# Kernel optimization log

Hardware: AMD Instinct MI355X
Metric: run time of the kernel (lower is better)

## Reference

```python
import jax, jax.numpy as jnp
import numpy as np
from jax.scipy.linalg import solve_triangular

B, T, HID = 1, 2048, 2048
HK, DK = 16, 96
HV, DV = 16, 192
KDIM, VDIM = HK * DK, HV * DV
KCONV = 4
CHUNK = 64
EPS = 1e-6


def setup_inputs():
    key = jax.random.key(0)
    ks = jax.random.split(key, 16)
    s = 0.02
    return {
        "hidden_states": jax.random.normal(ks[0], (B, T, HID), jnp.float32),
        "Wq": jax.random.normal(ks[1], (HID, KDIM), jnp.float32) * s,
        "Wk": jax.random.normal(ks[2], (HID, KDIM), jnp.float32) * s,
        "Wv": jax.random.normal(ks[3], (HID, VDIM), jnp.float32) * s,
        "Wb": jax.random.normal(ks[4], (HID, HV), jnp.float32) * s,
        "Wa": jax.random.normal(ks[5], (HID, HV), jnp.float32) * s,
        "Wg": jax.random.normal(ks[6], (HID, VDIM), jnp.float32) * s,
        "Wo": jax.random.normal(ks[7], (VDIM, HID), jnp.float32) * s,
        "conv_q": jax.random.normal(ks[8], (KDIM, KCONV), jnp.float32) * 0.5,
        "conv_k": jax.random.normal(ks[9], (KDIM, KCONV), jnp.float32) * 0.5,
        "conv_v": jax.random.normal(ks[10], (VDIM, KCONV), jnp.float32) * 0.5,
        "A_log": jnp.log(jax.random.uniform(ks[11], (HV,), jnp.float32, 1.0, 16.0)),
        "dt_bias": jax.random.uniform(ks[12], (HV,), jnp.float32, 0.0, 1.0),
        "norm_weight": jnp.ones((DV,), jnp.float32),
    }


def short_conv_silu(x, w):
    # x: [B,T,C], w: [C,K]; causal depthwise conv (left pad K-1) then SiLU
    K = w.shape[-1]
    xp = jnp.pad(x, ((0, 0), (K - 1, 0), (0, 0)))
    y = sum(xp[:, j:j + x.shape[1], :] * w[:, j] for j in range(K))
    return jax.nn.silu(y)


def l2norm(x):
    return x * jax.lax.rsqrt(jnp.sum(x * x, axis=-1, keepdims=True) + EPS)


def chunk_gated_delta_rule(q, k, v, g, beta):
    # q,k: [B,T,H,dk]; v: [B,T,H,dv]; g,beta: [B,T,H]. Chunked parallel scan (WY form).
    Bb, Tt, H, dk = q.shape
    dv = v.shape[-1]
    N = Tt // CHUNK
    q = l2norm(q) * (dk ** -0.5)
    k = l2norm(k)
    chunk = lambda x: x.transpose(0, 2, 1, 3).reshape(Bb, H, N, CHUNK, x.shape[-1])
    qc, kc, vc = chunk(q), chunk(k), chunk(v)
    gc = jnp.cumsum(g.transpose(0, 2, 1).reshape(Bb, H, N, CHUNK), axis=-1)
    bc = beta.transpose(0, 2, 1).reshape(Bb, H, N, CHUNK)

    m_inc = jnp.tril(jnp.ones((CHUNK, CHUNK), bool))
    m_str = jnp.tril(jnp.ones((CHUNK, CHUNK), bool), -1)
    diff = gc[..., :, None] - gc[..., None, :]
    D = jnp.exp(jnp.where(m_inc, diff, 0.0)) * m_inc  # [B,H,N,C,C] intra-chunk decay

    kb = kc * bc[..., None]
    A = -jnp.einsum('bhnik,bhnjk->bhnij', kb, kc) * D * m_str
    eye = jnp.eye(CHUNK, dtype=q.dtype)
    # UT transform: Tm = (I - A)^{-1}, A strictly lower triangular
    Tm = solve_triangular(eye - A, jnp.broadcast_to(eye, A.shape), lower=True, unit_diagonal=True)
    u = Tm @ (vc * bc[..., None])                   # [B,H,N,C,dv]
    w = Tm @ (kb * jnp.exp(gc)[..., None])          # [B,H,N,C,dk]
    g_last = gc[..., -1]                            # [B,H,N]

    def step(S, inp):
        q_i, k_i, u_i, w_i, g_i, D_i, gl = inp
        v_new = u_i - w_i @ S                       # [B,H,C,dv]
        attn = jnp.einsum('bhik,bhjk->bhij', q_i, k_i) * D_i
        o_i = (q_i * jnp.exp(g_i)[..., None]) @ S + attn @ v_new
        k_dec = k_i * jnp.exp(gl[..., None] - g_i)[..., None]
        S = S * jnp.exp(gl)[..., None, None] + jnp.einsum('bhck,bhcv->bhkv', k_dec, v_new)
        return S, o_i

    mv = lambda x: jnp.moveaxis(x, 2, 0)
    S0 = jnp.zeros((Bb, H, dk, dv), q.dtype)
    _, o = jax.lax.scan(step, S0, (mv(qc), mv(kc), mv(u), mv(w), mv(gc), mv(D), mv(g_last)))
    o = jnp.moveaxis(o, 0, 2).reshape(Bb, H, Tt, dv)
    return o.transpose(0, 2, 1, 3)                  # [B,T,H,dv]


def reference(hidden_states, Wq, Wk, Wv, Wb, Wa, Wg, Wo, conv_q, conv_k, conv_v, A_log, dt_bias, norm_weight):
    q = short_conv_silu(hidden_states @ Wq, conv_q).reshape(B, T, HK, DK)
    k = short_conv_silu(hidden_states @ Wk, conv_k).reshape(B, T, HK, DK)
    v = short_conv_silu(hidden_states @ Wv, conv_v).reshape(B, T, HV, DV)
    beta = jax.nn.sigmoid(hidden_states @ Wb) * 2.0          # allow_neg_eigval -> beta in [0,2]
    g = -jnp.exp(A_log) * jax.nn.softplus(hidden_states @ Wa + dt_bias)  # log decay, [B,T,HV]
    o = chunk_gated_delta_rule(q, k, v, g, beta)             # [B,T,HV,DV]
    gate = (hidden_states @ Wg).reshape(B, T, HV, DV)
    o = o * jax.nn.silu(gate)                                # gated RMSNorm (gate, then norm)
    o = o * jax.lax.rsqrt(jnp.mean(o * o, axis=-1, keepdims=True) + EPS) * norm_weight
    return o.reshape(B, T, VDIM) @ Wo
```

## Files before the change

### kernel.cpp

```cpp
#include <hip/hip_runtime.h>
#include <math.h>

#define T_LEN 2048
#define HIDN  2048
#define HKN   16
#define DKN   96
#define HVN   16
#define DVN   192
#define KDIMN 1536
#define VDIMN 3072
#define QKVD  6144
#define CHUNKN 64
#define NCHUNK 32
#define EPSF 1e-6f
#define TN_STRIDE 10240

typedef __attribute__((ext_vector_type(8))) short short8;
typedef __attribute__((ext_vector_type(4))) float f32x4;

__device__ __forceinline__ unsigned short f2bf(float f) {
    unsigned int u = __float_as_uint(f);
    unsigned int r = (u + 0x7FFFu + ((u >> 16) & 1u)) >> 16;
    return (unsigned short)r;
}
__device__ __forceinline__ float bf2f(unsigned short u) {
    return __uint_as_float(((unsigned int)u) << 16);
}
__device__ __forceinline__ float siluf(float x) { return x / (1.f + expf(-x)); }

__device__ __forceinline__ void gld_lds16(const void* g, void* l) {
    __builtin_amdgcn_global_load_lds((const __attribute__((address_space(1))) unsigned int*)g,
                                     (__attribute__((address_space(3))) unsigned int*)l, 16, 0, 0);
}

__global__ void cast_f32_bf16(const float* __restrict__ in, unsigned short* __restrict__ out, int n) {
    int i = (blockIdx.x * blockDim.x + threadIdx.x) * 4;
    if (i >= n) return;
    float4 v = *(const float4*)(in + i);
    ushort4 o;
    o.x = f2bf(v.x); o.y = f2bf(v.y); o.z = f2bf(v.z); o.w = f2bf(v.w);
    *(ushort4*)(out + i) = o;
}

__global__ void prep_weights(const float* __restrict__ Wq, const float* __restrict__ Wk,
                             const float* __restrict__ Wv, const float* __restrict__ Wg,
                             const float* __restrict__ Wo,
                             unsigned short* __restrict__ WallT, unsigned short* __restrict__ WoT) {
    __shared__ float tile[64][65];
    int bid = blockIdx.x;
    const float* W; unsigned short* Wt; int K, N, l;
    if (bid < 768)       { W = Wq; Wt = WallT;                          K = 2048; N = 1536; l = bid; }
    else if (bid < 1536) { W = Wk; Wt = WallT + (size_t)1536 * 2048;    K = 2048; N = 1536; l = bid - 768; }
    else if (bid < 3072) { W = Wv; Wt = WallT + (size_t)3072 * 2048;    K = 2048; N = 3072; l = bid - 1536; }
    else if (bid < 4608) { W = Wg; Wt = WallT + (size_t)6144 * 2048;    K = 2048; N = 3072; l = bid - 3072; }
    else                 { W = Wo; Wt = WoT;                            K = 3072; N = 2048; l = bid - 4608; }
    int nbx = N >> 6;
    int n0 = (l % nbx) * 64, k0 = (l / nbx) * 64;
    int tx = threadIdx.x, ty = threadIdx.y;
    for (int r = ty; r < 64; r += 4) tile[r][tx] = W[(size_t)(k0 + r) * N + n0 + tx];
    __syncthreads();
    for (int r = ty; r < 64; r += 4) Wt[(size_t)(n0 + r) * K + k0 + tx] = f2bf(tile[tx][r]);
}

__global__ __launch_bounds__(256) void gemm_bt2(const unsigned short* __restrict__ A,
                                                const unsigned short* __restrict__ Bt,
                                                float* __restrict__ C1, int ld1, int nblk1,
                                                unsigned short* __restrict__ C2, int ld2,
                                                int M, int K) {
    __shared__ __align__(16) unsigned short As[2][128 * 32];
    __shared__ __align__(16) unsigned short Bs[2][128 * 32];
    int tid = threadIdx.x;
    int wave = tid >> 6, lane = tid & 63;
    int bm = blockIdx.y, bn = blockIdx.x;
    f32x4 acc[4][4] = {};
    int wr = wave >> 1, wc = wave & 1;
    int rstage = wave * 32 + (lane >> 2);
    int cstage = (lane & 3) * 8;
    const size_t a_row0 = (size_t)bm * 128;
    const size_t b_row0 = (size_t)bn * 128;
    const unsigned short* gaBase = A + (a_row0 + rstage) * (size_t)K + cstage;
    const unsigned short* gbBase = Bt + (b_row0 + rstage) * (size_t)K + cstage;
    int row_a[4], row_b[4];
#pragma unroll
    for (int i = 0; i < 4; ++i) {
        row_a[i] = wr * 64 + i * 16 + (lane & 15);
        row_b[i] = wc * 64 + i * 16 + (lane & 15);
    }
    int koff = (lane >> 4) * 8;
    int niter = K >> 5;
    {
        unsigned short* ab = &As[0][wave * 1024];
        unsigned short* bb = &Bs[0][wave * 1024];
        gld_lds16(gaBase, ab);
        gld_lds16(gaBase + (size_t)16 * K, ab + 512);
        gld_lds16(gbBase, bb);
        gld_lds16(gbBase + (size_t)16 * K, bb + 512);
    }
    __syncthreads();
    for (int i = 0; i < niter; ++i) {
        int cur = i & 1;
        if (i + 1 < niter) {
            int k0 = (i + 1) * 32;
            unsigned short* ab = &As[cur ^ 1][wave * 1024];
            unsigned short* bb = &Bs[cur ^ 1][wave * 1024];
            gld_lds16(gaBase + k0, ab);
            gld_lds16(gaBase + k0 + (size_t)16 * K, ab + 512);
            gld_lds16(gbBase + k0, bb);
            gld_lds16(gbBase + k0 + (size_t)16 * K, bb + 512);
        }
        short8 af[4], bfr[4];
#pragma unroll
        for (int mi = 0; mi < 4; ++mi) af[mi] = *(const short8*)&As[cur][row_a[mi] * 32 + koff];
#pragma unroll
        for (int ni = 0; ni < 4; ++ni) bfr[ni] = *(const short8*)&Bs[cur][row_b[ni] * 32 + koff];
#pragma unroll
        for (int mi = 0; mi < 4; ++mi)
#pragma unroll
            for (int ni = 0; ni < 4; ++ni)
                acc[mi][ni] = __builtin_amdgcn_mfma_f32_16x16x32_bf16(af[mi], bfr[ni], acc[mi][ni], 0, 0, 0);
        __syncthreads();
    }
    if (bn < nblk1) {
        int colb = bn * 128;
#pragma unroll
        for (int mi = 0; mi < 4; ++mi) {
            int rbase = bm * 128 + wr * 64 + mi * 16 + (lane >> 4) * 4;
#pragma unroll
            for (int ni = 0; ni < 4; ++ni) {
                int col = colb + wc * 64 + ni * 16 + (lane & 15);
#pragma unroll
                for (int j = 0; j < 4; ++j)
                    C1[(size_t)(rbase + j) * ld1 + col] = acc[mi][ni][j];
            }
        }
    } else {
        int colb = (bn - nblk1) * 128;
#pragma unroll
        for (int mi = 0; mi < 4; ++mi) {
            int rbase = bm * 128 + wr * 64 + mi * 16 + (lane >> 4) * 4;
#pragma unroll
            for (int ni = 0; ni < 4; ++ni) {
                int col = colb + wc * 64 + ni * 16 + (lane & 15);
#pragma unroll
                for (int j = 0; j < 4; ++j)
                    C2[(size_t)(rbase + j) * ld2 + col] = f2bf(acc[mi][ni][j]);
            }
        }
    }
}

__global__ __launch_bounds__(256) void gemm_btk(const unsigned short* __restrict__ A,
                                                const unsigned short* __restrict__ Bt,
                                                float* __restrict__ C, float* __restrict__ Cp,
                                                int M, int N, int K) {
    __shared__ __align__(16) unsigned short As[2][128 * 32];
    __shared__ __align__(16) unsigned short Bs[2][128 * 32];
    int tid = threadIdx.x;
    int wave = tid >> 6, lane = tid & 63;
    int bm = blockIdx.y, bn = blockIdx.x, kz = blockIdx.z;
    int kchunk = K / 3;
    int kbeg = kz * kchunk;
    f32x4 acc[4][4] = {};
    int wr = wave >> 1, wc = wave & 1;
    int rstage = wave * 32 + (lane >> 2);
    int cstage = (lane & 3) * 8;
    const size_t a_row0 = (size_t)bm * 128;
    const size_t b_row0 = (size_t)bn * 128;
    const unsigned short* gaBase = A + (a_row0 + rstage) * (size_t)K + kbeg + cstage;
    const unsigned short* gbBase = Bt + (b_row0 + rstage) * (size_t)K + kbeg + cstage;
    int row_a[4], row_b[4];
#pragma unroll
    for (int i = 0; i < 4; ++i) {
        row_a[i] = wr * 64 + i * 16 + (lane & 15);
        row_b[i] = wc * 64 + i * 16 + (lane & 15);
    }
    int koff = (lane >> 4) * 8;
    int niter = kchunk >> 5;
    {
        unsigned short* ab = &As[0][wave * 1024];
        unsigned short* bb = &Bs[0][wave * 1024];
        gld_lds16(gaBase, ab);
        gld_lds16(gaBase + (size_t)16 * K, ab + 512);
        gld_lds16(gbBase, bb);
        gld_lds16(gbBase + (size_t)16 * K, bb + 512);
    }
    __syncthreads();
    for (int i = 0; i < niter; ++i) {
        int cur = i & 1;
        if (i + 1 < niter) {
            int k0 = (i + 1) * 32;
            unsigned short* ab = &As[cur ^ 1][wave * 1024];
            unsigned short* bb = &Bs[cur ^ 1][wave * 1024];
            gld_lds16(gaBase + k0, ab);
            gld_lds16(gaBase + k0 + (size_t)16 * K, ab + 512);
            gld_lds16(gbBase + k0, bb);
            gld_lds16(gbBase + k0 + (size_t)16 * K, bb + 512);
        }
        short8 af[4], bfr[4];
#pragma unroll
        for (int mi = 0; mi < 4; ++mi) af[mi] = *(const short8*)&As[cur][row_a[mi] * 32 + koff];
#pragma unroll
        for (int ni = 0; ni < 4; ++ni) bfr[ni] = *(const short8*)&Bs[cur][row_b[ni] * 32 + koff];
#pragma unroll
        for (int mi = 0; mi < 4; ++mi)
#pragma unroll
            for (int ni = 0; ni < 4; ++ni)
                acc[mi][ni] = __builtin_amdgcn_mfma_f32_16x16x32_bf16(af[mi], bfr[ni], acc[mi][ni], 0, 0, 0);
        __syncthreads();
    }
    float* Cout = (kz == 0) ? C : (Cp + (size_t)(kz - 1) * M * N);
#pragma unroll
    for (int mi = 0; mi < 4; ++mi) {
        int rbase = bm * 128 + wr * 64 + mi * 16 + (lane >> 4) * 4;
#pragma unroll
        for (int ni = 0; ni < 4; ++ni) {
            int col = bn * 128 + wc * 64 + ni * 16 + (lane & 15);
#pragma unroll
            for (int j = 0; j < 4; ++j)
                Cout[(size_t)(rbase + j) * N + col] = acc[mi][ni][j];
        }
    }
}

__global__ void addk(float* __restrict__ out, const float* __restrict__ p, int n) {
    int i = (blockIdx.x * blockDim.x + threadIdx.x) * 4;
    if (i >= n) return;
    float4 a = *(const float4*)(out + i);
    float4 b = *(const float4*)(p + i);
    float4 c = *(const float4*)(p + n + i);
    a.x += b.x + c.x; a.y += b.y + c.y; a.z += b.z + c.z; a.w += b.w + c.w;
    *(float4*)(out + i) = a;
}

__global__ __launch_bounds__(256) void beta_g(const float* __restrict__ X,
                                              const float* __restrict__ Wb, const float* __restrict__ Wa,
                                              const float* __restrict__ A_log, const float* __restrict__ dtb,
                                              float* __restrict__ bvec, float* __restrict__ gvec) {
    int t = blockIdx.x;
    int tid = threadIdx.x;
    int cg = tid & 7, ks = tid >> 3;
    int wave = tid >> 6, lane = tid & 63;
    const float* xr = X + (size_t)t * HIDN;
    const float* Wsel = (cg < 4) ? Wb : Wa;
    int cc = (cg & 3) * 4;
    float ax = 0.f, ay = 0.f, az = 0.f, aw = 0.f;
#pragma unroll 4
    for (int i = 0; i < 16; ++i) {
        int k = (ks + 32 * i) * 4;
        float4 xv = *(const float4*)(xr + k);
        float4 w0 = *(const float4*)(Wsel + (size_t)(k + 0) * 16 + cc);
        float4 w1 = *(const float4*)(Wsel + (size_t)(k + 1) * 16 + cc);
        float4 w2 = *(const float4*)(Wsel + (size_t)(k + 2) * 16 + cc);
        float4 w3 = *(const float4*)(Wsel + (size_t)(k + 3) * 16 + cc);
        ax += xv.x * w0.x + xv.y * w1.x + xv.z * w2.x + xv.w * w3.x;
        ay += xv.x * w0.y + xv.y * w1.y + xv.z * w2.y + xv.w * w3.y;
        az += xv.x * w0.z + xv.y * w1.z + xv.z * w2.z + xv.w * w3.z;
        aw += xv.x * w0.w + xv.y * w1.w + xv.z * w2.w + xv.w * w3.w;
    }
#pragma unroll
    for (int off = 8; off <= 32; off <<= 1) {
        ax += __shfl_xor(ax, off, 64);
        ay += __shfl_xor(ay, off, 64);
        az += __shfl_xor(az, off, 64);
        aw += __shfl_xor(aw, off, 64);
    }
    __shared__ float red[4][8][4];
    if ((lane >> 3) == 0) {
        red[wave][cg][0] = ax; red[wave][cg][1] = ay;
        red[wave][cg][2] = az; red[wave][cg][3] = aw;
    }
    __syncthreads();
    if (tid < 8) {
        float tot[4];
#pragma unroll
        for (int j = 0; j < 4; ++j)
            tot[j] = red[0][tid][j] + red[1][tid][j] + red[2][tid][j] + red[3][tid][j];
        int c0 = (tid & 3) * 4;
        if (tid < 4) {
#pragma unroll
            for (int j = 0; j < 4; ++j)
                bvec[(size_t)t * 16 + c0 + j] = 2.f / (1.f + expf(-tot[j]));
        } else {
#pragma unroll
            for (int j = 0; j < 4; ++j) {
                float a = tot[j] + dtb[c0 + j];
                float sp = (a > 20.f) ? a : log1pf(expf(a));
                gvec[(size_t)t * 16 + c0 + j] = -expf(A_log[c0 + j]) * sp;
            }
        }
    }
}

__global__ __launch_bounds__(256) void phase1_mfma(
    const float* __restrict__ Cqkv,
    const float* __restrict__ cq, const float* __restrict__ ck, const float* __restrict__ cv,
    const float* __restrict__ gvec, const float* __restrict__ bvec,
    float* __restrict__ u_ws, float* __restrict__ w_ws,
    float* __restrict__ qg_ws, float* __restrict__ at_ws,
    float* __restrict__ gl_ws, float* __restrict__ Ct,
    unsigned short* __restrict__ Tn) {
    int n = blockIdx.x, h = blockIdx.y;
    int t0 = n * CHUNKN;
    int tid = threadIdx.x;
    int wave = tid >> 6, lane = tid & 63;
    size_t base = (size_t)(h * NCHUNK + n);

    __shared__ __align__(16) char LB1[139776];
    unsigned short* QKb  = (unsigned short*)(LB1 + 0);
    unsigned short* Pb   = (unsigned short*)(LB1 + 26624);
    unsigned short* RHSw = (unsigned short*)(LB1 + 39936);
    unsigned short* RHSv = (unsigned short*)(LB1 + 53760);
    unsigned short* Ab   = (unsigned short*)(LB1 + 81408);
    unsigned short* Atb  = (unsigned short*)(LB1 + 94720);
    unsigned short* Ptb  = (unsigned short*)(LB1 + 108032);
    float*          Pf   = (float*)(LB1 + 121344);
    unsigned short* kdT  = (unsigned short*)(LB1 + 81408);
    unsigned short* wT   = (unsigned short*)(LB1 + 95232);
    unsigned short* uT   = (unsigned short*)(LB1 + 109056);
    float* gr_s = (float*)(LB1 + 138752);
    float* gc_s = gr_s + 64;
    float* be_s = gc_s + 64;
    float* egc  = be_s + 64;
    __shared__ __align__(16) float cwS[384 * 4];

    for (int f = tid; f < 384; f += 256) {
        const float* src = (f < 96)  ? (cq + (size_t)(h * 96 + f) * 4)
                         : (f < 192) ? (ck + (size_t)(h * 96 + f - 96) * 4)
                                     : (cv + (size_t)(h * 192 + f - 192) * 4);
        *(float4*)&cwS[f * 4] = *(const float4*)src;
    }
    if (tid < 64) {
        gr_s[tid] = gvec[(size_t)(t0 + tid) * HVN + h];
        be_s[tid] = bvec[(size_t)(t0 + tid) * HVN + h];
    }
    __syncthreads();
    if (tid < 64) {
        float sacc = 0.f;
        for (int j = 0; j <= tid; ++j) sacc += gr_s[j];
        gc_s[tid] = sacc;
    }
    __syncthreads();
    float gl = gc_s[63];
    if (tid < 64) egc[tid] = expf(gl - gc_s[tid]);

    int r = tid >> 2, sub = tid & 3;
    int trow = t0 + r;
    {
        int gc0 = 1536 + h * DKN + sub * 24;
        int lc0 = 96 + sub * 24;
        float kreg[24];
        float ss = 0.f;
#pragma unroll
        for (int i = 0; i < 6; ++i) {
            float4 x0 = (trow >= 3) ? *(const float4*)(Cqkv + (size_t)(trow - 3) * QKVD + gc0 + i * 4) : make_float4(0, 0, 0, 0);
            float4 x1 = (trow >= 2) ? *(const float4*)(Cqkv + (size_t)(trow - 2) * QKVD + gc0 + i * 4) : make_float4(0, 0, 0, 0);
            float4 x2 = (trow >= 1) ? *(const float4*)(Cqkv + (size_t)(trow - 1) * QKVD + gc0 + i * 4) : make_float4(0, 0, 0, 0);
            float4 x3 = *(const float4*)(Cqkv + (size_t)trow * QKVD + gc0 + i * 4);
#pragma unroll
            for (int c = 0; c < 4; ++c) {
                float4 w = *(const float4*)&cwS[(lc0 + i * 4 + c) * 4];
                float xv = ((const float*)&x0)[c] * w.x + ((const float*)&x1)[c] * w.y
                         + ((const float*)&x2)[c] * w.z + ((const float*)&x3)[c] * w.w;
                xv = siluf(xv);
                kreg[i * 4 + c] = xv;
                ss += xv * xv;
            }
        }
        ss += __shfl_xor(ss, 1, 64);
        ss += __shfl_xor(ss, 2, 64);
        float nrm = rsqrtf(ss + EPSF);
        float ebg = be_s[r] * expf(gc_s[r]);
#pragma unroll
        for (int i = 0; i < 24; ++i) {
            float kn = kreg[i] * nrm;
            QKb[r * 104 + sub * 24 + i] = f2bf(kn);
            RHSw[(sub * 24 + i) * 72 + r] = f2bf(kn * ebg);
        }
    }
    {
        int gc0 = h * DKN + sub * 24;
        int lc0 = sub * 24;
        float qreg[24];
        float ss = 0.f;
#pragma unroll
        for (int i = 0; i < 6; ++i) {
            float4 x0 = (trow >= 3) ? *(const float4*)(Cqkv + (size_t)(trow - 3) * QKVD + gc0 + i * 4) : make_float4(0, 0, 0, 0);
            float4 x1 = (trow >= 2) ? *(const float4*)(Cqkv + (size_t)(trow - 2) * QKVD + gc0 + i * 4) : make_float4(0, 0, 0, 0);
            float4 x2 = (trow >= 1) ? *(const float4*)(Cqkv + (size_t)(trow - 1) * QKVD + gc0 + i * 4) : make_float4(0, 0, 0, 0);
            float4 x3 = *(const float4*)(Cqkv + (size_t)trow * QKVD + gc0 + i * 4);
#pragma unroll
            for (int c = 0; c < 4; ++c) {
                float4 w = *(const float4*)&cwS[(lc0 + i * 4 + c) * 4];
                float xv = ((const float*)&x0)[c] * w.x + ((const float*)&x1)[c] * w.y
                         + ((const float*)&x2)[c] * w.z + ((const float*)&x3)[c] * w.w;
                xv = siluf(xv);
                qreg[i * 4 + c] = xv;
                ss += xv * xv;
            }
        }
        ss += __shfl_xor(ss, 1, 64);
        ss += __shfl_xor(ss, 2, 64);
        float nrm = rsqrtf(ss + EPSF) * 0.10206207261596577f;
        float eg = expf(gc_s[r]);
        float* qgp = qg_ws + base * (64 * 96) + r * 96 + sub * 24;
#pragma unroll
        for (int i = 0; i < 24; ++i) {
            float qn = qreg[i] * nrm;
            QKb[(64 + r) * 104 + sub * 24 + i] = f2bf(qn);
            qgp[i] = qn * eg;
        }
    }
    {
        int gc0 = 3072 + h * DVN + sub * 48;
        int lc0 = 192 + sub * 48;
        float ber = be_s[r];
#pragma unroll
        for (int i = 0; i < 12; ++i) {
            float4 x0 = (trow >= 3) ? *(const float4*)(Cqkv + (size_t)(trow - 3) * QKVD + gc0 + i * 4) : make_float4(0, 0, 0, 0);
            float4 x1 = (trow >= 2) ? *(const float4*)(Cqkv + (size_t)(trow - 2) * QKVD + gc0 + i * 4) : make_float4(0, 0, 0, 0);
            float4 x2 = (trow >= 1) ? *(const float4*)(Cqkv + (size_t)(trow - 1) * QKVD + gc0 + i * 4) : make_float4(0, 0, 0, 0);
            float4 x3 = *(const float4*)(Cqkv + (size_t)trow * QKVD + gc0 + i * 4);
#pragma unroll
            for (int c = 0; c < 4; ++c) {
                float4 w = *(const float4*)&cwS[(lc0 + i * 4 + c) * 4];
                float xv = ((const float*)&x0)[c] * w.x + ((const float*)&x1)[c] * w.y
                         + ((const float*)&x2)[c] * w.z + ((const float*)&x3)[c] * w.w;
                RHSv[(sub * 48 + i * 4 + c) * 72 + r] = f2bf(siluf(xv) * ber);
            }
        }
    }
    __syncthreads();

    {
        f32x4 acc1[2][4] = {};
#pragma unroll
        for (int ks = 0; ks < 3; ++ks) {
            int ko = ks * 32 + (lane >> 4) * 8;
            short8 af[2], bfv[4];
#pragma unroll
            for (int rt2 = 0; rt2 < 2; ++rt2)
                af[rt2] = *(const short8*)&QKb[(wave * 32 + rt2 * 16 + (lane & 15)) * 104 + ko];
#pragma unroll
            for (int ct = 0; ct < 4; ++ct)
                bfv[ct] = *(const short8*)&QKb[(ct * 16 + (lane & 15)) * 104 + ko];
#pragma unroll
            for (int rt2 = 0; rt2 < 2; ++rt2)
#pragma unroll
                for (int ct = 0; ct < 4; ++ct)
                    acc1[rt2][ct] = __builtin_amdgcn_mfma_f32_16x16x32_bf16(af[rt2], bfv[ct], acc1[rt2][ct], 0, 0, 0);
        }
#pragma unroll
        for (int rt2 = 0; rt2 < 2; ++rt2)
#pragma unroll
            for (int ct = 0; ct < 4; ++ct)
#pragma unroll
                for (int j = 0; j < 4; ++j) {
                    int rr = wave * 32 + rt2 * 16 + (lane >> 4) * 4 + j;
                    int cc = ct * 16 + (lane & 15);
                    float val = acc1[rt2][ct][j];
                    if (rr < 64) {
                        float av = (rr > cc) ? -be_s[rr] * expf(gc_s[rr] - gc_s[cc]) * val : 0.f;
                        unsigned short ab = f2bf(av);
                        Ab[rr * 104 + cc] = ab;
                        Atb[cc * 104 + rr] = ab;
                        float pv = (rr == cc) ? 1.f : av;
                        Pf[rr * 68 + cc] = pv;
                        unsigned short pb = f2bf(pv);
                        Pb[rr * 104 + cc] = pb;
                        Ptb[cc * 104 + rr] = pb;
                    } else {
                        int ar = rr - 64;
                        float av = (ar >= cc) ? expf(gc_s[ar] - gc_s[cc]) * val : 0.f;
                        at_ws[base * (64 * 64) + ar * 64 + cc] = av;
                    }
                }
    }
    __syncthreads();

#pragma unroll 1
    for (int lev = 0; lev < 5; ++lev) {
        f32x4 d[4] = {};
#pragma unroll
        for (int ks = 0; ks < 2; ++ks) {
            int ko = ks * 32 + (lane >> 4) * 8;
            short8 a0 = *(const short8*)&Ab[(wave * 16 + (lane & 15)) * 104 + ko];
#pragma unroll
            for (int ct = 0; ct < 4; ++ct) {
                short8 b0 = *(const short8*)&Atb[(ct * 16 + (lane & 15)) * 104 + ko];
                d[ct] = __builtin_amdgcn_mfma_f32_16x16x32_bf16(a0, b0, d[ct], 0, 0, 0);
            }
        }
        __syncthreads();
#pragma unroll
        for (int ct = 0; ct < 4; ++ct)
#pragma unroll
            for (int j = 0; j < 4; ++j) {
                int rr = wave * 16 + (lane >> 4) * 4 + j;
                int cc = ct * 16 + (lane & 15);
                unsigned short hb = f2bf(d[ct][j]);
                Ab[rr * 104 + cc] = hb;
                Atb[cc * 104 + rr] = hb;
            }
        __syncthreads();
        f32x4 e[4];
#pragma unroll
        for (int ct = 0; ct < 4; ++ct)
#pragma unroll
            for (int j = 0; j < 4; ++j)
                e[ct][j] = Pf[(wave * 16 + (lane >> 4) * 4 + j) * 68 + ct * 16 + (lane & 15)];
#pragma unroll
        for (int ks = 0; ks < 2; ++ks) {
            int ko = ks * 32 + (lane >> 4) * 8;
            short8 a0 = *(const short8*)&Ab[(wave * 16 + (lane & 15)) * 104 + ko];
#pragma unroll
            for (int ct = 0; ct < 4; ++ct) {
                short8 b0 = *(const short8*)&Ptb[(ct * 16 + (lane & 15)) * 104 + ko];
                e[ct] = __builtin_amdgcn_mfma_f32_16x16x32_bf16(a0, b0, e[ct], 0, 0, 0);
            }
        }
        __syncthreads();
#pragma unroll
        for (int ct = 0; ct < 4; ++ct)
#pragma unroll
            for (int j = 0; j < 4; ++j) {
                int rr = wave * 16 + (lane >> 4) * 4 + j;
                int cc = ct * 16 + (lane & 15);
                float pv = e[ct][j];
                Pf[rr * 68 + cc] = pv;
                unsigned short pb = f2bf(pv);
                Pb[rr * 104 + cc] = pb;
                Ptb[cc * 104 + rr] = pb;
            }
        __syncthreads();
    }

    for (int f = tid; f < 6144; f += 256) {
        int d = f >> 6, tt = f & 63;
        kdT[d * 72 + tt] = f2bf(bf2f(QKb[tt * 104 + d]) * egc[tt]);
    }

#pragma unroll 1
    for (int i = 0; i < 18; ++i) {
        int id = wave * 18 + i;
        int rt = id & 3, ct = id >> 2;
        f32x4 o4 = {};
#pragma unroll
        for (int ks = 0; ks < 2; ++ks) {
            int ko = ks * 32 + (lane >> 4) * 8;
            short8 a0 = *(const short8*)&Pb[(rt * 16 + (lane & 15)) * 104 + ko];
            short8 b0 = (ct < 12)
                ? *(const short8*)&RHSv[(ct * 16 + (lane & 15)) * 72 + ko]
                : *(const short8*)&RHSw[((ct - 12) * 16 + (lane & 15)) * 72 + ko];
            o4 = __builtin_amdgcn_mfma_f32_16x16x32_bf16(a0, b0, o4, 0, 0, 0);
        }
#pragma unroll
        for (int j = 0; j < 4; ++j) {
            int rr = rt * 16 + (lane >> 4) * 4 + j;
            int nn = ct * 16 + (lane & 15);
            if (ct < 12) {
                u_ws[base * (64 * 192) + rr * 192 + nn] = o4[j];
                uT[nn * 72 + rr] = f2bf(o4[j]);
            } else {
                w_ws[base * (64 * 96) + rr * 96 + (nn - 192)] = o4[j];
                wT[(nn - 192) * 72 + rr] = f2bf(o4[j]);
            }
        }
    }
    __syncthreads();

    float eglv = expf(gl);
#pragma unroll 1
    for (int q = 0; q < 27; ++q) {
        int id = wave * 27 + q;
        f32x4 acc = {};
        if (id < 36) {
            int jt = id / 6, kt = id % 6;
#pragma unroll
            for (int ks = 0; ks < 2; ++ks) {
                int ko = ks * 32 + (lane >> 4) * 8;
                short8 a0 = *(const short8*)&kdT[(jt * 16 + (lane & 15)) * 72 + ko];
                short8 b0 = *(const short8*)&wT[(kt * 16 + (lane & 15)) * 72 + ko];
                acc = __builtin_amdgcn_mfma_f32_16x16x32_bf16(a0, b0, acc, 0, 0, 0);
            }
#pragma unroll
            for (int rr = 0; rr < 4; ++rr) {
                int j = jt * 16 + (lane >> 4) * 4 + rr;
                int k = kt * 16 + (lane & 15);
                float val = -acc[rr];
                if (j == k) val += eglv;
                Tn[base * TN_STRIDE + j * 104 + k] = f2bf(val);
            }
        } else {
            int cid = id - 36;
            int it = cid / 6, jt = cid % 6;
#pragma unroll
            for (int ks = 0; ks < 2; ++ks) {
                int ko = ks * 32 + (lane >> 4) * 8;
                short8 a0 = *(const short8*)&uT[(it * 16 + (lane & 15)) * 72 + ko];
                short8 b0 = *(const short8*)&kdT[(jt * 16 + (lane & 15)) * 72 + ko];
                acc = __builtin_amdgcn_mfma_f32_16x16x32_bf16(a0, b0, acc, 0, 0, 0);
            }
#pragma unroll
            for (int rr = 0; rr < 4; ++rr)
                Ct[base * 18432 + (size_t)(it * 16 + (lane >> 4) * 4 + rr) * 96 + jt * 16 + (lane & 15)] = acc[rr];
        }
    }
    if (tid == 0) gl_ws[base] = gl;
}

__global__ __launch_bounds__(128) void mscan(const float* __restrict__ Ct, const unsigned short* __restrict__ Tn,
                                             float* __restrict__ s_ws) {
    int rg = blockIdx.x, h = blockIdx.y;
    int tid = threadIdx.x, wave = tid >> 6, lane = tid & 63;
    __shared__ __align__(16) unsigned short St[48 * 104];
    __shared__ __align__(16) unsigned short TnB[2][TN_STRIDE];
    __shared__ __align__(16) float CtB[2][48 * 96];
    for (int i = tid; i < 48 * 104; i += 128) St[i] = 0;

    {
        const float* cp = Ct + (size_t)(h * NCHUNK) * 18432 + rg * (48 * 96);
        const unsigned short* tp = Tn + (size_t)(h * NCHUNK) * TN_STRIDE;
#pragma unroll
        for (int q = 0; q < 9; ++q) {
            size_t o = (size_t)(wave * 9 + q) * 1024 + lane * 16;
            gld_lds16((const char*)cp + o, (char*)&CtB[0][0] + (size_t)(wave * 9 + q) * 1024);
        }
#pragma unroll
        for (int q = 0; q < 10; ++q) {
            size_t o = (size_t)(wave * 10 + q) * 1024 + lane * 16;
            gld_lds16((const char*)tp + o, (char*)&TnB[0][0] + (size_t)(wave * 10 + q) * 1024);
        }
    }
    f32x4 acc[3][3] = {};
    int colw = wave * 48;
    __syncthreads();

#pragma unroll 1
    for (int n = 0; n < NCHUNK; ++n) {
        size_t base = (size_t)(h * NCHUNK + n);
        int cur = n & 1;
        if (n + 1 < NCHUNK) {
            const float* cp = Ct + (base + 1) * 18432 + rg * (48 * 96);
            const unsigned short* tp = Tn + (base + 1) * TN_STRIDE;
#pragma unroll
            for (int q = 0; q < 9; ++q) {
                size_t o = (size_t)(wave * 9 + q) * 1024 + lane * 16;
                gld_lds16((const char*)cp + o, (char*)&CtB[cur ^ 1][0] + (size_t)(wave * 9 + q) * 1024);
            }
#pragma unroll
            for (int q = 0; q < 10; ++q) {
                size_t o = (size_t)(wave * 10 + q) * 1024 + lane * 16;
                gld_lds16((const char*)tp + o, (char*)&TnB[cur ^ 1][0] + (size_t)(wave * 10 + q) * 1024);
            }
        }
        float* sp = s_ws + base * 18432 + rg * (48 * 96);
#pragma unroll
        for (int it = 0; it < 3; ++it)
#pragma unroll
            for (int jt = 0; jt < 3; ++jt) {
                int irow = it * 16 + (lane >> 4) * 4;
                int col = colw + jt * 16 + (lane & 15);
#pragma unroll
                for (int r = 0; r < 4; ++r) {
                    sp[(size_t)(irow + r) * 96 + col] = acc[it][jt][r];
                    acc[it][jt][r] = CtB[cur][(irow + r) * 96 + col];
                }
            }
#pragma unroll
        for (int ks = 0; ks < 3; ++ks) {
            int ko = ks * 32 + (lane >> 4) * 8;
            short8 af[3], bfv[3];
#pragma unroll
            for (int it = 0; it < 3; ++it)
                af[it] = *(const short8*)&St[(it * 16 + (lane & 15)) * 104 + ko];
#pragma unroll
            for (int jt = 0; jt < 3; ++jt)
                bfv[jt] = *(const short8*)&TnB[cur][(colw + jt * 16 + (lane & 15)) * 104 + ko];
#pragma unroll
            for (int it = 0; it < 3; ++it)
#pragma unroll
                for (int jt = 0; jt < 3; ++jt)
                    acc[it][jt] = __builtin_amdgcn_mfma_f32_16x16x32_bf16(af[it], bfv[jt], acc[it][jt], 0, 0, 0);
        }
        __syncthreads();
#pragma unroll
        for (int it = 0; it < 3; ++it)
#pragma unroll
            for (int jt = 0; jt < 3; ++jt)
#pragma unroll
                for (int r = 0; r < 4; ++r)
                    St[(it * 16 + (lane >> 4) * 4 + r) * 104 + colw + jt * 16 + (lane & 15)] = f2bf(acc[it][jt][r]);
        __syncthreads();
    }
}

#define P2_ST 0
#define P2_W  39936
#define P2_QG 53248
#define P2_AT 66560
#define P2_U  75776
#define P2_VN 125952
__global__ __launch_bounds__(256) void phase2b_mfma(const float* __restrict__ s_ws, const float* __restrict__ w_ws,
                                                    const float* __restrict__ qg_ws, const float* __restrict__ at_ws,
                                                    const float* __restrict__ u_ws,
                                                    const unsigned short* __restrict__ Cgate,
                                                    const float* __restrict__ nw,
                                                    unsigned short* __restrict__ obf) {
    __shared__ __align__(16) char LB[153600];
    unsigned short* StB = (unsigned short*)(LB + P2_ST);
    unsigned short* wB  = (unsigned short*)(LB + P2_W);
    unsigned short* qgB = (unsigned short*)(LB + P2_QG);
    unsigned short* atB = (unsigned short*)(LB + P2_AT);
    float* uF           = (float*)(LB + P2_U);
    unsigned short* vnB = (unsigned short*)(LB + P2_VN);
    int n = blockIdx.x, h = blockIdx.y;
    size_t base = (size_t)(h * NCHUNK + n);
    int tid = threadIdx.x, wave = tid >> 6, lane = tid & 63;
    int i0w = wave * 48;
    {
        const float* sp = s_ws + base * 18432;
        for (int f = tid; f < 4608; f += 256) {
            int i = f / 24, c4 = (f % 24) * 4;
            float4 v = *(const float4*)(sp + i * 96 + c4);
            ushort4 o4; o4.x = f2bf(v.x); o4.y = f2bf(v.y); o4.z = f2bf(v.z); o4.w = f2bf(v.w);
            *(ushort4*)&StB[i * 104 + c4] = o4;
        }
    }
    {
        const float* wp = w_ws + base * 6144;
        const float* qp = qg_ws + base * 6144;
        for (int f = tid; f < 1536; f += 256) {
            int t = f / 24, c4 = (f % 24) * 4;
            float4 wv = *(const float4*)(wp + t * 96 + c4);
            float4 qv = *(const float4*)(qp + t * 96 + c4);
            ushort4 ow; ow.x = f2bf(-wv.x); ow.y = f2bf(-wv.y); ow.z = f2bf(-wv.z); ow.w = f2bf(-wv.w);
            ushort4 oq; oq.x = f2bf(qv.x); oq.y = f2bf(qv.y); oq.z = f2bf(qv.z); oq.w = f2bf(qv.w);
            *(ushort4*)&wB[t * 104 + c4] = ow;
            *(ushort4*)&qgB[t * 104 + c4] = oq;
        }
    }
    {
        const float* ap = at_ws + base * 4096;
        for (int f = tid; f < 1024; f += 256) {
            int t = f / 16, c4 = (f % 16) * 4;
            float4 av = *(const float4*)(ap + t * 64 + c4);
            ushort4 oa; oa.x = f2bf(av.x); oa.y = f2bf(av.y); oa.z = f2bf(av.z); oa.w = f2bf(av.w);
            *(ushort4*)&atB[t * 72 + c4] = oa;
        }
    }
    {
        const float* up = u_ws + base * 12288;
        for (int f = tid; f < 3072; f += 256) {
            int t = f / 48, c4 = (f % 48) * 4;
            *(float4*)&uF[t * 196 + c4] = *(const float4*)(up + t * 192 + c4);
        }
    }
    __syncthreads();
    {
        f32x4 acc[3][4];
#pragma unroll
        for (int it = 0; it < 3; ++it)
#pragma unroll
            for (int jt = 0; jt < 4; ++jt)
#pragma unroll
                for (int r = 0; r < 4; ++r)
                    acc[it][jt][r] = uF[(jt * 16 + (lane & 15)) * 196 + i0w + it * 16 + (lane >> 4) * 4 + r];
#pragma unroll
        for (int ks = 0; ks < 3; ++ks) {
            int ko = ks * 32 + (lane >> 4) * 8;
            short8 af[3], bfv[4];
#pragma unroll
            for (int it = 0; it < 3; ++it)
                af[it] = *(const short8*)&StB[(i0w + it * 16 + (lane & 15)) * 104 + ko];
#pragma unroll
            for (int jt = 0; jt < 4; ++jt)
                bfv[jt] = *(const short8*)&wB[(jt * 16 + (lane & 15)) * 104 + ko];
#pragma unroll
            for (int it = 0; it < 3; ++it)
#pragma unroll
                for (int jt = 0; jt < 4; ++jt)
                    acc[it][jt] = __builtin_amdgcn_mfma_f32_16x16x32_bf16(af[it], bfv[jt], acc[it][jt], 0, 0, 0);
        }
#pragma unroll
        for (int it = 0; it < 3; ++it)
#pragma unroll
            for (int jt = 0; jt < 4; ++jt)
#pragma unroll
                for (int r = 0; r < 4; ++r)
                    vnB[(i0w + it * 16 + (lane >> 4) * 4 + r) * 72 + jt * 16 + (lane & 15)] = f2bf(acc[it][jt][r]);
    }
    f32x4 acc2[3][4] = {};
#pragma unroll
    for (int ks = 0; ks < 3; ++ks) {
        int ko = ks * 32 + (lane >> 4) * 8;
        short8 af[3], bfv[4];
#pragma unroll
        for (int it = 0; it < 3; ++it)
            af[it] = *(const short8*)&StB[(i0w + it * 16 + (lane & 15)) * 104 + ko];
#pragma unroll
        for (int jt = 0; jt < 4; ++jt)
            bfv[jt] = *(const short8*)&qgB[(jt * 16 + (lane & 15)) * 104 + ko];
#pragma unroll
        for (int it = 0; it < 3; ++it)
#pragma unroll
            for (int jt = 0; jt < 4; ++jt)
                acc2[it][jt] = __builtin_amdgcn_mfma_f32_16x16x32_bf16(af[it], bfv[jt], acc2[it][jt], 0, 0, 0);
    }
#pragma unroll
    for (int ks = 0; ks < 2; ++ks) {
        int ko = ks * 32 + (lane >> 4) * 8;
        short8 af[3], bfv[4];
#pragma unroll
        for (int it = 0; it < 3; ++it)
            af[it] = *(const short8*)&vnB[(i0w + it * 16 + (lane & 15)) * 72 + ko];
#pragma unroll
        for (int jt = 0; jt < 4; ++jt)
            bfv[jt] = *(const short8*)&atB[(jt * 16 + (lane & 15)) * 72 + ko];
#pragma unroll
        for (int it = 0; it < 3; ++it)
#pragma unroll
            for (int jt = 0; jt < 4; ++jt)
                acc2[it][jt] = __builtin_amdgcn_mfma_f32_16x16x32_bf16(af[it], bfv[jt], acc2[it][jt], 0, 0, 0);
    }
    __syncthreads();
    float* oF = (float*)(LB + 0);
#pragma unroll
    for (int it = 0; it < 3; ++it)
#pragma unroll
        for (int jt = 0; jt < 4; ++jt)
#pragma unroll
            for (int r = 0; r < 4; ++r)
                oF[(i0w + it * 16 + (lane >> 4) * 4 + r) * 68 + jt * 16 + (lane & 15)] = acc2[it][jt][r];
    __syncthreads();

    float* ssq = (float*)(LB + 131072);
    float* rno = (float*)(LB + 132096);
    int jj = tid >> 2, qq = tid & 3;
    int t0 = n * CHUNKN;
    {
        const unsigned short* gp = Cgate + (size_t)(t0 + jj) * VDIMN + h * DVN + qq * 48;
        float ss = 0.f;
#pragma unroll 4
        for (int m = 0; m < 48; ++m) {
            int i = qq * 48 + m;
            float x = oF[i * 68 + jj];
            float g = bf2f(gp[m]);
            float xv = x * siluf(g);
            oF[i * 68 + jj] = xv;
            ss += xv * xv;
        }
        ssq[jj * 4 + qq] = ss;
    }
    __syncthreads();
    if (tid < 64) {
        float tot = ssq[tid * 4] + ssq[tid * 4 + 1] + ssq[tid * 4 + 2] + ssq[tid * 4 + 3];
        rno[tid] = rsqrtf(tot * (1.f / 192.f) + EPSF);
    }
    __syncthreads();
    {
        float rr2 = rno[jj];
        unsigned short* op = obf + (size_t)(t0 + jj) * VDIMN + h * DVN + qq * 48;
#pragma unroll 4
        for (int m = 0; m < 48; ++m) {
            int i = qq * 48 + m;
            op[m] = f2bf(oF[i * 68 + jj] * rr2 * nw[i]);
        }
    }
}

extern "C" void kernel_launch(void* const* d_in, const int* in_sizes, int n_in,
                              void* d_out, int out_size, void* d_ws, size_t ws_size,
                              hipStream_t stream) {
    (void)in_sizes; (void)n_in; (void)out_size;
    const float* X    = (const float*)d_in[0];
    const float* Wq   = (const float*)d_in[1];
    const float* Wk   = (const float*)d_in[2];
    const float* Wv   = (const float*)d_in[3];
    const float* Wb   = (const float*)d_in[4];
    const float* Wa   = (const float*)d_in[5];
    const float* Wg   = (const float*)d_in[6];
    const float* Wo   = (const float*)d_in[7];
    const float* cq   = (const float*)d_in[8];
    const float* ck   = (const float*)d_in[9];
    const float* cv   = (const float*)d_in[10];
    const float* Alog = (const float*)d_in[11];
    const float* dtb  = (const float*)d_in[12];
    const float* nw   = (const float*)d_in[13];

    const size_t OFF_XBF   = 0;
    const size_t OFF_WALLT = 8388608;
    const size_t OFF_WOT   = 46137344;
    const size_t OFF_CQKV  = 58720256;
    const size_t OFF_CGATE = 109051904;
    const size_t OFF_CT    = 134217728;
    const size_t OFF_TN    = OFF_CT + 37748736;
    const size_t OFF_GVEC  = 184549376;
    const size_t OFF_BVEC  = 184680448;
    const size_t OFF_GL    = 184811520;
    const size_t OFF_U     = 184819712;
    const size_t OFF_W     = 209985536;
    const size_t OFF_QG    = 222568448;
    const size_t OFF_AT    = OFF_XBF;
    const size_t OFF_S     = OFF_CQKV;
    const size_t OFF_OBF   = OFF_WALLT + 25165824;
    const size_t OFF_OPART = OFF_CQKV;
    const size_t NEEDED    = 235151360;
    if (ws_size < NEEDED) return;

    char* ws = (char*)d_ws;
    unsigned short* Xbf   = (unsigned short*)(ws + OFF_XBF);
    unsigned short* WallT = (unsigned short*)(ws + OFF_WALLT);
    unsigned short* WoT   = (unsigned short*)(ws + OFF_WOT);
    float* Cqkv  = (float*)(ws + OFF_CQKV);
    unsigned short* Cgate = (unsigned short*)(ws + OFF_CGATE);
    float* gvec  = (float*)(ws + OFF_GVEC);
    float* bvec  = (float*)(ws + OFF_BVEC);
    float* gl_ws = (float*)(ws + OFF_GL);
    float* u_ws  = (float*)(ws + OFF_U);
    float* w_ws  = (float*)(ws + OFF_W);
    float* qg_ws = (float*)(ws + OFF_QG);
    float* at_ws = (float*)(ws + OFF_AT);
    float* Ct    = (float*)(ws + OFF_CT);
    unsigned short* Tn = (unsigned short*)(ws + OFF_TN);
    float* s_ws  = (float*)(ws + OFF_S);
    unsigned short* obf = (unsigned short*)(ws + OFF_OBF);
    float* opart = (float*)(ws + OFF_OPART);

    cast_f32_bf16<<<4096, 256, 0, stream>>>(X, Xbf, 2048 * 2048);
    prep_weights<<<6144, dim3(64, 4), 0, stream>>>(Wq, Wk, Wv, Wg, Wo, WallT, WoT);

    gemm_bt2<<<dim3(9216 / 128, 2048 / 128), 256, 0, stream>>>(Xbf, WallT,
                                                               Cqkv, QKVD, QKVD / 128,
                                                               Cgate, VDIMN, 2048, 2048);

    beta_g<<<T_LEN, 256, 0, stream>>>(X, Wb, Wa, Alog, dtb, bvec, gvec);

    phase1_mfma<<<dim3(NCHUNK, HVN), 256, 0, stream>>>(Cqkv, cq, ck, cv, gvec, bvec,
                                                       u_ws, w_ws, qg_ws, at_ws, gl_ws, Ct, Tn);
    mscan<<<dim3(4, HVN), 128, 0, stream>>>(Ct, Tn, s_ws);
    phase2b_mfma<<<dim3(NCHUNK, HVN), 256, 0, stream>>>(s_ws, w_ws, qg_ws, at_ws, u_ws,
                                                        Cgate, nw, obf);

    gemm_btk<<<dim3(2048 / 128, 2048 / 128, 3), 256, 0, stream>>>(obf, WoT, (float*)d_out, opart,
                                                                  2048, 2048, 3072);
    addk<<<4096, 256, 0, stream>>>((float*)d_out, opart, 2048 * 2048);
}
```

Before: 413.5 us.

## Store inter-phase workspaces in bf16 LDS-ready layout and fuse X cast into beta_g

The per-chunk intermediates (w, qg, A-tilde, Ct, and the scanned states S) are now written as bf16 in the padded row strides phase2b uses in LDS, so phase2b can load them with direct global-to-LDS copies instead of reading fp32 and converting. mscan now writes the bf16 state tile straight from LDS rather than spilling fp32 accumulators. The standalone f32-to-bf16 cast of X is folded into beta_g, and the unused gl_ws output is dropped. This cuts workspace traffic and a kernel launch, but Ct is now rounded to bf16 before the scan accumulates it, which may add error.

```diff
diff --git a/kernel.cpp b/kernel.cpp
--- a/kernel.cpp
+++ b/kernel.cpp
@@ -14,6 +14,11 @@
 #define NCHUNK 32
 #define EPSF 1e-6f
 #define TN_STRIDE 10240
+#define WQG_ST 6656
+#define AT_ST  4608
+#define CT_ST  18432
+#define S_ST   19968
+#define U_ST   12288
 
 typedef __attribute__((ext_vector_type(8))) short short8;
 typedef __attribute__((ext_vector_type(4))) float f32x4;
@@ -31,15 +36,6 @@
 __device__ __forceinline__ void gld_lds16(const void* g, void* l) {
     __builtin_amdgcn_global_load_lds((const __attribute__((address_space(1))) unsigned int*)g,
                                      (__attribute__((address_space(3))) unsigned int*)l, 16, 0, 0);
-}
-
-__global__ void cast_f32_bf16(const float* __restrict__ in, unsigned short* __restrict__ out, int n) {
-    int i = (blockIdx.x * blockDim.x + threadIdx.x) * 4;
-    if (i >= n) return;
-    float4 v = *(const float4*)(in + i);
-    ushort4 o;
-    o.x = f2bf(v.x); o.y = f2bf(v.y); o.z = f2bf(v.z); o.w = f2bf(v.w);
-    *(ushort4*)(out + i) = o;
 }
 
 __global__ void prep_weights(const float* __restrict__ Wq, const float* __restrict__ Wk,
@@ -235,7 +231,8 @@
 __global__ __launch_bounds__(256) void beta_g(const float* __restrict__ X,
                                               const float* __restrict__ Wb, const float* __restrict__ Wa,
                                               const float* __restrict__ A_log, const float* __restrict__ dtb,
-                                              float* __restrict__ bvec, float* __restrict__ gvec) {
+                                              float* __restrict__ bvec, float* __restrict__ gvec,
+                                              unsigned short* __restrict__ Xbf) {
     int t = blockIdx.x;
     int tid = threadIdx.x;
     int cg = tid & 7, ks = tid >> 3;
@@ -248,6 +245,11 @@
     for (int i = 0; i < 16; ++i) {
         int k = (ks + 32 * i) * 4;
         float4 xv = *(const float4*)(xr + k);
+        if (cg == 0) {
+            ushort4 xo;
+            xo.x = f2bf(xv.x); xo.y = f2bf(xv.y); xo.z = f2bf(xv.z); xo.w = f2bf(xv.w);
+            *(ushort4*)(Xbf + (size_t)t * HIDN + k) = xo;
+        }
         float4 w0 = *(const float4*)(Wsel + (size_t)(k + 0) * 16 + cc);
         float4 w1 = *(const float4*)(Wsel + (size_t)(k + 1) * 16 + cc);
         float4 w2 = *(const float4*)(Wsel + (size_t)(k + 2) * 16 + cc);
@@ -295,10 +297,9 @@
     const float* __restrict__ Cqkv,
     const float* __restrict__ cq, const float* __restrict__ ck, const float* __restrict__ cv,
     const float* __restrict__ gvec, const float* __restrict__ bvec,
-    float* __restrict__ u_ws, float* __restrict__ w_ws,
-    float* __restrict__ qg_ws, float* __restrict__ at_ws,
-    float* __restrict__ gl_ws, float* __restrict__ Ct,
-    unsigned short* __restrict__ Tn) {
+    float* __restrict__ u_ws, unsigned short* __restrict__ w_bf,
+    unsigned short* __restrict__ qg_bf, unsigned short* __restrict__ at_bf,
+    unsigned short* __restrict__ Ct, unsigned short* __restrict__ Tn) {
     int n = blockIdx.x, h = blockIdx.y;
     int t0 = n * CHUNKN;
     int tid = threadIdx.x;
@@ -402,12 +403,12 @@
         ss += __shfl_xor(ss, 2, 64);
         float nrm = rsqrtf(ss + EPSF) * 0.10206207261596577f;
         float eg = expf(gc_s[r]);
-        float* qgp = qg_ws + base * (64 * 96) + r * 96 + sub * 24;
+        unsigned short* qgp = qg_bf + base * WQG_ST + r * 104 + sub * 24;
 #pragma unroll
         for (int i = 0; i < 24; ++i) {
             float qn = qreg[i] * nrm;
             QKb[(64 + r) * 104 + sub * 24 + i] = f2bf(qn);
-            qgp[i] = qn * eg;
+            qgp[i] = f2bf(qn * eg);
         }
     }
     {
@@ -471,7 +472,7 @@
                     } else {
                         int ar = rr - 64;
                         float av = (ar >= cc) ? expf(gc_s[ar] - gc_s[cc]) * val : 0.f;
-                        at_ws[base * (64 * 64) + ar * 64 + cc] = av;
+                        at_bf[base * AT_ST + ar * 72 + cc] = f2bf(av);
                     }
                 }
     }
@@ -533,7 +534,6 @@
             }
         __syncthreads();
     }
-
     for (int f = tid; f < 6144; f += 256) {
         int d = f >> 6, tt = f & 63;
         kdT[d * 72 + tt] = f2bf(bf2f(QKb[tt * 104 + d]) * egc[tt]);
@@ -558,10 +558,10 @@
             int rr = rt * 16 + (lane >> 4) * 4 + j;
             int nn = ct * 16 + (lane & 15);
             if (ct < 12) {
-                u_ws[base * (64 * 192) + rr * 192 + nn] = o4[j];
+                u_ws[base * U_ST + rr * 192 + nn] = o4[j];
                 uT[nn * 72 + rr] = f2bf(o4[j]);
             } else {
-                w_ws[base * (64 * 96) + rr * 96 + (nn - 192)] = o4[j];
+                w_bf[base * WQG_ST + rr * 104 + (nn - 192)] = f2bf(-o4[j]);
                 wT[(nn - 192) * 72 + rr] = f2bf(o4[j]);
             }
         }
@@ -602,36 +602,33 @@
             }
 #pragma unroll
             for (int rr = 0; rr < 4; ++rr)
-                Ct[base * 18432 + (size_t)(it * 16 + (lane >> 4) * 4 + rr) * 96 + jt * 16 + (lane & 15)] = acc[rr];
-        }
-    }
-    if (tid == 0) gl_ws[base] = gl;
-}
-
-__global__ __launch_bounds__(128) void mscan(const float* __restrict__ Ct, const unsigned short* __restrict__ Tn,
-                                             float* __restrict__ s_ws) {
+                Ct[base * CT_ST + (size_t)(it * 16 + (lane >> 4) * 4 + rr) * 96 + jt * 16 + (lane & 15)] = f2bf(acc[rr]);
+        }
+    }
+}
+
+__global__ __launch_bounds__(128) void mscan(const unsigned short* __restrict__ Ct,
+                                             const unsigned short* __restrict__ Tn,
+                                             unsigned short* __restrict__ s_bf) {
     int rg = blockIdx.x, h = blockIdx.y;
     int tid = threadIdx.x, wave = tid >> 6, lane = tid & 63;
     __shared__ __align__(16) unsigned short St[48 * 104];
     __shared__ __align__(16) unsigned short TnB[2][TN_STRIDE];
-    __shared__ __align__(16) float CtB[2][48 * 96];
+    __shared__ __align__(16) unsigned short CtB[2][48 * 96];
     for (int i = tid; i < 48 * 104; i += 128) St[i] = 0;
 
     {
-        const float* cp = Ct + (size_t)(h * NCHUNK) * 18432 + rg * (48 * 96);
-        const unsigned short* tp = Tn + (size_t)(h * NCHUNK) * TN_STRIDE;
-#pragma unroll
-        for (int q = 0; q < 9; ++q) {
-            size_t o = (size_t)(wave * 9 + q) * 1024 + lane * 16;
-            gld_lds16((const char*)cp + o, (char*)&CtB[0][0] + (size_t)(wave * 9 + q) * 1024);
-        }
+        const char* cp = (const char*)(Ct + (size_t)(h * NCHUNK) * CT_ST + rg * (48 * 96));
+        const char* tp = (const char*)(Tn + (size_t)(h * NCHUNK) * TN_STRIDE);
+        for (int q = wave; q < 9; q += 2)
+            gld_lds16(cp + (size_t)q * 1024 + lane * 16, (char*)&CtB[0][0] + (size_t)q * 1024);
 #pragma unroll
         for (int q = 0; q < 10; ++q) {
             size_t o = (size_t)(wave * 10 + q) * 1024 + lane * 16;
-            gld_lds16((const char*)tp + o, (char*)&TnB[0][0] + (size_t)(wave * 10 + q) * 1024);
-        }
-    }
-    f32x4 acc[3][3] = {};
+            gld_lds16(tp + o, (char*)&TnB[0][0] + (size_t)(wave * 10 + q) * 1024);
+        }
+    }
+    f32x4 acc[3][3];
     int colw = wave * 48;
     __syncthreads();
 
@@ -640,20 +637,21 @@
         size_t base = (size_t)(h * NCHUNK + n);
         int cur = n & 1;
         if (n + 1 < NCHUNK) {
-            const float* cp = Ct + (base + 1) * 18432 + rg * (48 * 96);
-            const unsigned short* tp = Tn + (base + 1) * TN_STRIDE;
-#pragma unroll
-            for (int q = 0; q < 9; ++q) {
-                size_t o = (size_t)(wave * 9 + q) * 1024 + lane * 16;
-                gld_lds16((const char*)cp + o, (char*)&CtB[cur ^ 1][0] + (size_t)(wave * 9 + q) * 1024);
-            }
+            const char* cp = (const char*)(Ct + (base + 1) * CT_ST + rg * (48 * 96));
+            const char* tp = (const char*)(Tn + (base + 1) * TN_STRIDE);
+            for (int q = wave; q < 9; q += 2)
+                gld_lds16(cp + (size_t)q * 1024 + lane * 16, (char*)&CtB[cur ^ 1][0] + (size_t)q * 1024);
 #pragma unroll
             for (int q = 0; q < 10; ++q) {
                 size_t o = (size_t)(wave * 10 + q) * 1024 + lane * 16;
-                gld_lds16((const char*)tp + o, (char*)&TnB[cur ^ 1][0] + (size_t)(wave * 10 + q) * 1024);
-            }
-        }
-        float* sp = s_ws + base * 18432 + rg * (48 * 96);
+                gld_lds16(tp + o, (char*)&TnB[cur ^ 1][0] + (size_t)(wave * 10 + q) * 1024);
+            }
+        }
+        {
+            unsigned short* sp = s_bf + base * S_ST + rg * 4992;
+            for (int f = tid; f < 624; f += 128)
+                *(short8*)(sp + f * 8) = *(const short8*)&St[f * 8];
+        }
 #pragma unroll
         for (int it = 0; it < 3; ++it)
 #pragma unroll
@@ -661,10 +659,8 @@
                 int irow = it * 16 + (lane >> 4) * 4;
                 int col = colw + jt * 16 + (lane & 15);
 #pragma unroll
-                for (int r = 0; r < 4; ++r) {
-                    sp[(size_t)(irow + r) * 96 + col] = acc[it][jt][r];
-                    acc[it][jt][r] = CtB[cur][(irow + r) * 96 + col];
-                }
+                for (int r = 0; r < 4; ++r)
+                    acc[it][jt][r] = bf2f(CtB[cur][(irow + r) * 96 + col]);
             }
 #pragma unroll
         for (int ks = 0; ks < 3; ++ks) {
@@ -700,8 +696,10 @@
 #define P2_AT 66560
 #define P2_U  75776
 #define P2_VN 125952
-__global__ __launch_bounds__(256) void phase2b_mfma(const float* __restrict__ s_ws, const float* __restrict__ w_ws,
-                                                    const float* __restrict__ qg_ws, const float* __restrict__ at_ws,
+__global__ __launch_bounds__(256) void phase2b_mfma(const unsigned short* __restrict__ s_bf,
+                                                    const unsigned short* __restrict__ w_bf,
+                                                    const unsigned short* __restrict__ qg_bf,
+                                                    const unsigned short* __restrict__ at_bf,
                                                     const float* __restrict__ u_ws,
                                                     const unsigned short* __restrict__ Cgate,
                                                     const float* __restrict__ nw,
@@ -718,38 +716,21 @@
     int tid = threadIdx.x, wave = tid >> 6, lane = tid & 63;
     int i0w = wave * 48;
     {
-        const float* sp = s_ws + base * 18432;
-        for (int f = tid; f < 4608; f += 256) {
-            int i = f / 24, c4 = (f % 24) * 4;
-            float4 v = *(const float4*)(sp + i * 96 + c4);
-            ushort4 o4; o4.x = f2bf(v.x); o4.y = f2bf(v.y); o4.z = f2bf(v.z); o4.w = f2bf(v.w);
-            *(ushort4*)&StB[i * 104 + c4] = o4;
-        }
-    }
-    {
-        const float* wp = w_ws + base * 6144;
-        const float* qp = qg_ws + base * 6144;
-        for (int f = tid; f < 1536; f += 256) {
-            int t = f / 24, c4 = (f % 24) * 4;
-            float4 wv = *(const float4*)(wp + t * 96 + c4);
-            float4 qv = *(const float4*)(qp + t * 96 + c4);
-            ushort4 ow; ow.x = f2bf(-wv.x); ow.y = f2bf(-wv.y); ow.z = f2bf(-wv.z); ow.w = f2bf(-wv.w);
-            ushort4 oq; oq.x = f2bf(qv.x); oq.y = f2bf(qv.y); oq.z = f2bf(qv.z); oq.w = f2bf(qv.w);
-            *(ushort4*)&wB[t * 104 + c4] = ow;
-            *(ushort4*)&qgB[t * 104 + c4] = oq;
-        }
-    }
-    {
-        const float* ap = at_ws + base * 4096;
-        for (int f = tid; f < 1024; f += 256) {
-            int t = f / 16, c4 = (f % 16) * 4;
-            float4 av = *(const float4*)(ap + t * 64 + c4);
-            ushort4 oa; oa.x = f2bf(av.x); oa.y = f2bf(av.y); oa.z = f2bf(av.z); oa.w = f2bf(av.w);
-            *(ushort4*)&atB[t * 72 + c4] = oa;
-        }
-    }
-    {
-        const float* up = u_ws + base * 12288;
+        const char* sp = (const char*)(s_bf + base * S_ST);
+        const char* wp = (const char*)(w_bf + base * WQG_ST);
+        const char* qp = (const char*)(qg_bf + base * WQG_ST);
+        const char* ap = (const char*)(at_bf + base * AT_ST);
+        for (int q = wave; q < 39; q += 4)
+            gld_lds16(sp + (size_t)q * 1024 + lane * 16, LB + P2_ST + (size_t)q * 1024);
+        for (int q = wave; q < 13; q += 4)
+            gld_lds16(wp + (size_t)q * 1024 + lane * 16, LB + P2_W + (size_t)q * 1024);
+        for (int q = wave; q < 13; q += 4)
+            gld_lds16(qp + (size_t)q * 1024 + lane * 16, LB + P2_QG + (size_t)q * 1024);
+        for (int q = wave; q < 9; q += 4)
+            gld_lds16(ap + (size_t)q * 1024 + lane * 16, LB + P2_AT + (size_t)q * 1024);
+    }
+    {
+        const float* up = u_ws + base * U_ST;
         for (int f = tid; f < 3072; f += 256) {
             int t = f / 48, c4 = (f % 48) * 4;
             *(float4*)&uF[t * 196 + c4] = *(const float4*)(up + t * 192 + c4);
@@ -896,7 +877,6 @@
     const size_t OFF_TN    = OFF_CT + 37748736;
     const size_t OFF_GVEC  = 184549376;
     const size_t OFF_BVEC  = 184680448;
-    const size_t OFF_GL    = 184811520;
     const size_t OFF_U     = 184819712;
     const size_t OFF_W     = 209985536;
     const size_t OFF_QG    = 222568448;
@@ -915,30 +895,27 @@
     unsigned short* Cgate = (unsigned short*)(ws + OFF_CGATE);
     float* gvec  = (float*)(ws + OFF_GVEC);
     float* bvec  = (float*)(ws + OFF_BVEC);
-    float* gl_ws = (float*)(ws + OFF_GL);
     float* u_ws  = (float*)(ws + OFF_U);
-    float* w_ws  = (float*)(ws + OFF_W);
-    float* qg_ws = (float*)(ws + OFF_QG);
-    float* at_ws = (float*)(ws + OFF_AT);
-    float* Ct    = (float*)(ws + OFF_CT);
-    unsigned short* Tn = (unsigned short*)(ws + OFF_TN);
-    float* s_ws  = (float*)(ws + OFF_S);
-    unsigned short* obf = (unsigned short*)(ws + OFF_OBF);
+    unsigned short* w_bf  = (unsigned short*)(ws + OFF_W);
+    unsigned short* qg_bf = (unsigned short*)(ws + OFF_QG);
+    unsigned short* at_bf = (unsigned short*)(ws + OFF_AT);
+    unsigned short* Ct    = (unsigned short*)(ws + OFF_CT);
+    unsigned short* Tn    = (unsigned short*)(ws + OFF_TN);
+    unsigned short* s_bf  = (unsigned short*)(ws + OFF_S);
+    unsigned short* obf   = (unsigned short*)(ws + OFF_OBF);
     float* opart = (float*)(ws + OFF_OPART);
 
-    cast_f32_bf16<<<4096, 256, 0, stream>>>(X, Xbf, 2048 * 2048);
+    beta_g<<<T_LEN, 256, 0, stream>>>(X, Wb, Wa, Alog, dtb, bvec, gvec, Xbf);
     prep_weights<<<6144, dim3(64, 4), 0, stream>>>(Wq, Wk, Wv, Wg, Wo, WallT, WoT);
 
     gemm_bt2<<<dim3(9216 / 128, 2048 / 128), 256, 0, stream>>>(Xbf, WallT,
                                                                Cqkv, QKVD, QKVD / 128,
                                                                Cgate, VDIMN, 2048, 2048);
 
-    beta_g<<<T_LEN, 256, 0, stream>>>(X, Wb, Wa, Alog, dtb, bvec, gvec);
-
     phase1_mfma<<<dim3(NCHUNK, HVN), 256, 0, stream>>>(Cqkv, cq, ck, cv, gvec, bvec,
-                                                       u_ws, w_ws, qg_ws, at_ws, gl_ws, Ct, Tn);
-    mscan<<<dim3(4, HVN), 128, 0, stream>>>(Ct, Tn, s_ws);
-    phase2b_mfma<<<dim3(NCHUNK, HVN), 256, 0, stream>>>(s_ws, w_ws, qg_ws, at_ws, u_ws,
+                                                       u_ws, w_bf, qg_bf, at_bf, Ct, Tn);
+    mscan<<<dim3(4, HVN), 128, 0, stream>>>(Ct, Tn, s_bf);
+    phase2b_mfma<<<dim3(NCHUNK, HVN), 256, 0, stream>>>(s_bf, w_bf, qg_bf, at_bf, u_ws,
                                                         Cgate, nw, obf);
 
     gemm_btk<<<dim3(2048 / 128, 2048 / 128, 3), 256, 0, stream>>>(obf, WoT, (float*)d_out, opart,
```

Result: faster. 402.7 us (-2.6%).
